# Kernel tuning notes

Measured on AMD Instinct MI355X. Metric: run time of the kernel, lower is better.

The kernel has to match this reference:

```python
import jax, jax.numpy as jnp
import numpy as np

N_NODES = 100000
N_EDGES = 3200000
FEAT = 64
N_GRAPHS = 64


def setup_inputs() -> dict:
    key = jax.random.key(0)
    ks = jax.random.split(key, 6)
    x = jax.random.normal(ks[0], (N_NODES, FEAT), dtype=jnp.float32)
    edge_index = jax.random.randint(ks[1], (2, N_EDGES), 0, N_NODES, dtype=jnp.int64)
    batch = jnp.sort(jax.random.randint(ks[2], (N_NODES,), 0, N_GRAPHS, dtype=jnp.int64))
    W1 = jax.random.normal(ks[3], (FEAT, FEAT), dtype=jnp.float32) * 0.1
    b1 = jnp.zeros((FEAT,), dtype=jnp.float32)
    W2 = jax.random.normal(ks[4], (FEAT, FEAT), dtype=jnp.float32) * 0.1
    b2 = jnp.zeros((FEAT,), dtype=jnp.float32)
    return {"x": x, "edge_index": edge_index, "batch": batch,
            "W1": W1, "b1": b1, "W2": W2, "b2": b2}


def _gcn_conv(x, W, b, row, col, n_nodes):
    # GCNConv: x' = D^{-1/2} (A + I) D^{-1/2} (x W) + b  (self-loops already in row/col)
    h = x @ W                                               # [N, F_out]
    deg = jax.ops.segment_sum(jnp.ones_like(col, dtype=h.dtype), col,
                              num_segments=n_nodes)         # [N]
    dinv = jnp.where(deg > 0, jax.lax.rsqrt(deg), 0.0)
    norm = dinv[row] * dinv[col]                            # [E+N]
    msgs = h[row] * norm[:, None]                           # gather + scale  [E+N, F]
    out = jax.ops.segment_sum(msgs, col, num_segments=n_nodes)  # scatter-add
    return out + b


def reference(x, edge_index, batch, W1, b1, W2, b2):
    n_nodes = x.shape[0]
    # add self-loops (PyG GCNConv default)
    loop = jnp.arange(n_nodes, dtype=edge_index.dtype)
    row = jnp.concatenate([edge_index[0], loop])
    col = jnp.concatenate([edge_index[1], loop])

    h = _gcn_conv(x, W1, b1, row, col, n_nodes)
    h = jax.nn.relu(h)
    # dropout is identity in eval mode (deterministic reference)
    h = _gcn_conv(h, W2, b2, row, col, n_nodes)
    h = jax.nn.relu(h)

    # global mean pool over graphs in the batch
    sums = jax.ops.segment_sum(h, batch, num_segments=N_GRAPHS)          # [G, F]
    counts = jax.ops.segment_sum(jnp.ones((n_nodes,), h.dtype), batch,
                                 num_segments=N_GRAPHS)                  # [G]
    return sums / jnp.maximum(counts, 1.0)[:, None]
```

## Files before the change

kernel.cpp:

```cpp
#include <hip/hip_runtime.h>

#define N_NODES 100000
#define N_EDGES 3200000
#define FEAT 64
#define N_GRAPHS 64

#define BKT_SHIFT 8
#define BKT_SIZE  256
#define NBKT      391
#define BKT_PAD   8960
#define E4        (N_EDGES / 4)
#define GEMM1_BLKS ((N_NODES + 63) / 64)

__device__ __forceinline__ ushort f2bf(float f) {
    unsigned u = __float_as_uint(f);
    return (ushort)((u + 0x7fffu + ((u >> 16) & 1u)) >> 16);
}
__device__ __forceinline__ float bf2f(ushort s) {
    return __uint_as_float(((unsigned)s) << 16);
}

__global__ void k_zero(int* __restrict__ bcnt, float* __restrict__ pool, int* __restrict__ offs) {
    int i = blockIdx.x * blockDim.x + threadIdx.x;
    if (i < NBKT) bcnt[i] = 0;
    if (i < N_GRAPHS * FEAT + N_GRAPHS) pool[i] = 0.0f;
    if (i == 0) offs[N_NODES] = N_EDGES;
}

__global__ void __launch_bounds__(1024) k_pre(const int* __restrict__ row,
                                              const int* __restrict__ col,
                                              int* __restrict__ bcnt,
                                              int* __restrict__ tmp,
                                              const float* __restrict__ x,
                                              const float* __restrict__ W1,
                                              ushort* __restrict__ hbf) {
    __shared__ int lcnt0[NBKT];
    __shared__ int lcnt1[NBKT];
    __shared__ float Ws[64][64];
    __shared__ float At[64][68];
    int tid = threadIdx.x;

    if (blockIdx.x < 196) {
        int* lc = (tid >= 512) ? lcnt1 : lcnt0;
        if (tid < NBKT) { lcnt0[tid] = 0; lcnt1[tid] = 0; }
        __syncthreads();
        int base = blockIdx.x * 4096;
        int4 c[4];
        #pragma unroll
        for (int k = 0; k < 4; ++k) {
            int t4 = base + k * 1024 + tid;
            if (t4 < E4) {
                c[k] = ((const int4*)col)[t4];
                atomicAdd(&lc[c[k].x >> BKT_SHIFT], 1);
                atomicAdd(&lc[c[k].y >> BKT_SHIFT], 1);
                atomicAdd(&lc[c[k].z >> BKT_SHIFT], 1);
                atomicAdd(&lc[c[k].w >> BKT_SHIFT], 1);
            }
        }
        __syncthreads();
        if (tid < NBKT) {
            int l0 = lcnt0[tid], l1 = lcnt1[tid];
            int bse = atomicAdd(&bcnt[tid], l0 + l1);
            lcnt0[tid] = bse;
            lcnt1[tid] = bse + l0;
        }
        __syncthreads();
        #pragma unroll
        for (int k = 0; k < 4; ++k) {
            int t4 = base + k * 1024 + tid;
            if (t4 < E4) {
                int4 r = ((const int4*)row)[t4];
                int b0 = c[k].x >> BKT_SHIFT, b1 = c[k].y >> BKT_SHIFT;
                int b2 = c[k].z >> BKT_SHIFT, b3 = c[k].w >> BKT_SHIFT;
                int s0 = atomicAdd(&lc[b0], 1);
                int s1 = atomicAdd(&lc[b1], 1);
                int s2 = atomicAdd(&lc[b2], 1);
                int s3 = atomicAdd(&lc[b3], 1);
                if (s0 < BKT_PAD) tmp[b0 * BKT_PAD + s0] = (r.x << BKT_SHIFT) | (c[k].x & (BKT_SIZE - 1));
                if (s1 < BKT_PAD) tmp[b1 * BKT_PAD + s1] = (r.y << BKT_SHIFT) | (c[k].y & (BKT_SIZE - 1));
                if (s2 < BKT_PAD) tmp[b2 * BKT_PAD + s2] = (r.z << BKT_SHIFT) | (c[k].z & (BKT_SIZE - 1));
                if (s3 < BKT_PAD) tmp[b3 * BKT_PAD + s3] = (r.w << BKT_SHIFT) | (c[k].w & (BKT_SIZE - 1));
            }
        }
    } else {
        int row0 = (blockIdx.x - 196) * 64;
        {
            float4 v = ((const float4*)W1)[tid];
            *(float4*)&Ws[tid >> 4][(tid & 15) * 4] = v;
        }
        {
            int r = tid >> 4, f4 = tid & 15;
            int grow = row0 + r;
            float4 v = make_float4(0.f, 0.f, 0.f, 0.f);
            if (grow < N_NODES) v = ((const float4*)(x + (size_t)grow * FEAT))[f4];
            int k = f4 * 4;
            At[k][r] = v.x; At[k + 1][r] = v.y; At[k + 2][r] = v.z; At[k + 3][r] = v.w;
        }
        __syncthreads();
        int tx = tid & 31, ty = tid >> 5;
        float a00 = 0.f, a01 = 0.f, a10 = 0.f, a11 = 0.f;
        #pragma unroll 8
        for (int k = 0; k < 64; ++k) {
            float2 wv = *(const float2*)&Ws[k][tx * 2];
            float2 av = *(const float2*)&At[k][ty * 2];
            a00 = fmaf(av.x, wv.x, a00); a01 = fmaf(av.x, wv.y, a01);
            a10 = fmaf(av.y, wv.x, a10); a11 = fmaf(av.y, wv.y, a11);
        }
        int r0 = row0 + ty * 2;
        if (r0 < N_NODES)
            *(unsigned*)(hbf + (size_t)r0 * FEAT + tx * 2) =
                (unsigned)f2bf(a00) | ((unsigned)f2bf(a01) << 16);
        if (r0 + 1 < N_NODES)
            *(unsigned*)(hbf + (size_t)(r0 + 1) * FEAT + tx * 2) =
                (unsigned)f2bf(a10) | ((unsigned)f2bf(a11) << 16);
    }
}

__global__ void __launch_bounds__(1024) k_build(const int* __restrict__ tmp,
                                                const int* __restrict__ bcnt,
                                                int* __restrict__ offs,
                                                float* __restrict__ dinv,
                                                int* __restrict__ csr_row) {
    __shared__ int hist[BKT_SIZE];
    __shared__ int wpart[4];
    __shared__ int sh_start;
    int b = blockIdx.x, tid = threadIdx.x;

    if (tid < 64) {
        int sum = 0;
        for (int c = 0; c < NBKT; c += 64) {
            int idx = c + tid;
            int v = (idx < b) ? bcnt[idx] : 0;
            #pragma unroll
            for (int d2 = 1; d2 < 64; d2 <<= 1) v += __shfl_xor(v, d2);
            sum += v;
        }
        if (tid == 0) sh_start = sum;
    }
    if (tid < BKT_SIZE) hist[tid] = 0;
    __syncthreads();
    int s = sh_start;
    int count = min(bcnt[b], BKT_PAD);
    const int* seg = tmp + (size_t)b * BKT_PAD;

    int e[9];
    #pragma unroll
    for (int k = 0; k < 9; ++k) {
        int idx = k * 1024 + tid;
        e[k] = -1;
        if (idx < count) {
            e[k] = seg[idx];
            atomicAdd(&hist[e[k] & (BKT_SIZE - 1)], 1);
        }
    }
    __syncthreads();

    int cnt_n = 0, p = 0;
    if (tid < BKT_SIZE) {
        cnt_n = hist[tid];
        p = cnt_n;
        #pragma unroll
        for (int d = 1; d < 64; d <<= 1) {
            int t2 = __shfl_up(p, d);
            if ((tid & 63) >= d) p += t2;
        }
        if ((tid & 63) == 63) wpart[tid >> 6] = p;
    }
    __syncthreads();
    if (tid == 0) {
        int run = 0;
        #pragma unroll
        for (int w = 0; w < 4; ++w) { int t2 = wpart[w]; wpart[w] = run; run += t2; }
    }
    __syncthreads();
    if (tid < BKT_SIZE) {
        int excl = wpart[tid >> 6] + p - cnt_n;
        int node = (b << BKT_SHIFT) + tid;
        if (node < N_NODES) {
            offs[node] = s + excl;
            dinv[node] = rsqrtf((float)(cnt_n + 1));
        }
        hist[tid] = s + excl;
    }
    __syncthreads();

    #pragma unroll
    for (int k = 0; k < 9; ++k) {
        if (e[k] >= 0) {
            int slot = atomicAdd(&hist[e[k] & (BKT_SIZE - 1)], 1);
            csr_row[slot] = e[k] >> BKT_SHIFT;
        }
    }
}

__global__ void __launch_bounds__(256, 4) k_gemm2(const ushort* __restrict__ in,
                                                  const float* __restrict__ W,
                                                  const float* __restrict__ bias,
                                                  const float* __restrict__ dinv,
                                                  ushort* __restrict__ out) {
    __shared__ float Ws[64][64];
    __shared__ float At[64][68];
    int tid = threadIdx.x;
    int row0 = blockIdx.x * 64;

    const float4* Wv = (const float4*)W;
    #pragma unroll
    for (int i = 0; i < 4; ++i) {
        int idx = tid + i * 256;
        float4 v = Wv[idx];
        *(float4*)&Ws[idx >> 4][(idx & 15) * 4] = v;
    }
    #pragma unroll
    for (int i = 0; i < 2; ++i) {
        int idx = tid + i * 256;
        int r = idx >> 3, q = idx & 7;
        int grow = row0 + r;
        uint4 v = make_uint4(0u, 0u, 0u, 0u);
        if (grow < N_NODES) v = ((const uint4*)(in + (size_t)grow * FEAT))[q];
        float4 b0 = ((const float4*)bias)[q * 2];
        float4 b1 = ((const float4*)bias)[q * 2 + 1];
        int k = q * 8;
        At[k + 0][r] = fmaxf(__uint_as_float(v.x << 16)          + b0.x, 0.f);
        At[k + 1][r] = fmaxf(__uint_as_float(v.x & 0xffff0000u)  + b0.y, 0.f);
        At[k + 2][r] = fmaxf(__uint_as_float(v.y << 16)          + b0.z, 0.f);
        At[k + 3][r] = fmaxf(__uint_as_float(v.y & 0xffff0000u)  + b0.w, 0.f);
        At[k + 4][r] = fmaxf(__uint_as_float(v.z << 16)          + b1.x, 0.f);
        At[k + 5][r] = fmaxf(__uint_as_float(v.z & 0xffff0000u)  + b1.y, 0.f);
        At[k + 6][r] = fmaxf(__uint_as_float(v.w << 16)          + b1.z, 0.f);
        At[k + 7][r] = fmaxf(__uint_as_float(v.w & 0xffff0000u)  + b1.w, 0.f);
    }
    __syncthreads();

    int tx = tid & 15, ty = tid >> 4;
    float acc[4][4] = {};
    #pragma unroll 8
    for (int k = 0; k < 64; ++k) {
        float4 wv = *(const float4*)&Ws[k][tx * 4];
        float4 av = *(const float4*)&At[k][ty * 4];
        acc[0][0] = fmaf(av.x, wv.x, acc[0][0]); acc[0][1] = fmaf(av.x, wv.y, acc[0][1]);
        acc[0][2] = fmaf(av.x, wv.z, acc[0][2]); acc[0][3] = fmaf(av.x, wv.w, acc[0][3]);
        acc[1][0] = fmaf(av.y, wv.x, acc[1][0]); acc[1][1] = fmaf(av.y, wv.y, acc[1][1]);
        acc[1][2] = fmaf(av.y, wv.z, acc[1][2]); acc[1][3] = fmaf(av.y, wv.w, acc[1][3]);
        acc[2][0] = fmaf(av.z, wv.x, acc[2][0]); acc[2][1] = fmaf(av.z, wv.y, acc[2][1]);
        acc[2][2] = fmaf(av.z, wv.z, acc[2][2]); acc[2][3] = fmaf(av.z, wv.w, acc[2][3]);
        acc[3][0] = fmaf(av.w, wv.x, acc[3][0]); acc[3][1] = fmaf(av.w, wv.y, acc[3][1]);
        acc[3][2] = fmaf(av.w, wv.z, acc[3][2]); acc[3][3] = fmaf(av.w, wv.w, acc[3][3]);
    }
    #pragma unroll
    for (int i = 0; i < 4; ++i) {
        int r = row0 + ty * 4 + i;
        if (r < N_NODES) {
            float d = dinv[r];
            ushort4 o;
            o.x = f2bf(acc[i][0] * d);
            o.y = f2bf(acc[i][1] * d);
            o.z = f2bf(acc[i][2] * d);
            o.w = f2bf(acc[i][3] * d);
            *(ushort4*)(out + (size_t)r * FEAT + tx * 4) = o;
        }
    }
}

template <bool SRC_SCALED>
__global__ void k_gather(const ushort* __restrict__ h, const float* __restrict__ dinv,
                         const int* __restrict__ off, const int* __restrict__ csr_row,
                         ushort* __restrict__ out) {
    int tid = threadIdx.x;
    int lane = tid & 63;
    int node = blockIdx.x * (blockDim.x >> 6) + (tid >> 6);
    if (node >= N_NODES) return;
    int g = lane >> 3;
    int sl = lane & 7;
    int s = off[node], e = off[node + 1];
    float a0 = 0.f, a1 = 0.f, a2 = 0.f, a3 = 0.f, a4 = 0.f, a5 = 0.f, a6 = 0.f, a7 = 0.f;

#define ACC8(vv, wt) do {                                           \
        a0 = fmaf(__uint_as_float((vv).x << 16),         wt, a0);   \
        a1 = fmaf(__uint_as_float((vv).x & 0xffff0000u), wt, a1);   \
        a2 = fmaf(__uint_as_float((vv).y << 16),         wt, a2);   \
        a3 = fmaf(__uint_as_float((vv).y & 0xffff0000u), wt, a3);   \
        a4 = fmaf(__uint_as_float((vv).z << 16),         wt, a4);   \
        a5 = fmaf(__uint_as_float((vv).z & 0xffff0000u), wt, a5);   \
        a6 = fmaf(__uint_as_float((vv).w << 16),         wt, a6);   \
        a7 = fmaf(__uint_as_float((vv).w & 0xffff0000u), wt, a7);   \
    } while (0)

    float selfw = SRC_SCALED ? 1.0f : dinv[node];
    if (g == 0) {
        uint4 v = ((const uint4*)(h + (size_t)node * FEAT))[sl];
        ACC8(v, selfw);
    }
    int base = s;
    for (; base + 32 <= e; base += 32) {
        int r0 = csr_row[base + g];
        int r1 = csr_row[base + 8 + g];
        int r2 = csr_row[base + 16 + g];
        int r3 = csr_row[base + 24 + g];
        float w0 = SRC_SCALED ? 1.0f : dinv[r0];
        float w1 = SRC_SCALED ? 1.0f : dinv[r1];
        float w2 = SRC_SCALED ? 1.0f : dinv[r2];
        float w3 = SRC_SCALED ? 1.0f : dinv[r3];
        uint4 v0 = ((const uint4*)(h + (size_t)r0 * FEAT))[sl];
        uint4 v1 = ((const uint4*)(h + (size_t)r1 * FEAT))[sl];
        uint4 v2 = ((const uint4*)(h + (size_t)r2 * FEAT))[sl];
        uint4 v3 = ((const uint4*)(h + (size_t)r3 * FEAT))[sl];
        ACC8(v0, w0); ACC8(v1, w1); ACC8(v2, w2); ACC8(v3, w3);
    }
    if (base + 16 <= e) {
        int r0 = csr_row[base + g];
        int r1 = csr_row[base + 8 + g];
        float w0 = SRC_SCALED ? 1.0f : dinv[r0];
        float w1 = SRC_SCALED ? 1.0f : dinv[r1];
        uint4 v0 = ((const uint4*)(h + (size_t)r0 * FEAT))[sl];
        uint4 v1 = ((const uint4*)(h + (size_t)r1 * FEAT))[sl];
        ACC8(v0, w0); ACC8(v1, w1);
        base += 16;
    }
    for (; base < e; base += 8) {
        int ei = base + g;
        if (ei < e) {
            int r = csr_row[ei];
            float wt = SRC_SCALED ? 1.0f : dinv[r];
            uint4 v = ((const uint4*)(h + (size_t)r * FEAT))[sl];
            ACC8(v, wt);
        }
    }
#undef ACC8
#define RED(a) a += __shfl_xor(a, 8); a += __shfl_xor(a, 16); a += __shfl_xor(a, 32);
    RED(a0) RED(a1) RED(a2) RED(a3) RED(a4) RED(a5) RED(a6) RED(a7)
#undef RED
    if (g == 0) {
        float d = dinv[node];
        uint4 o;
        o.x = (unsigned)f2bf(a0 * d) | ((unsigned)f2bf(a1 * d) << 16);
        o.y = (unsigned)f2bf(a2 * d) | ((unsigned)f2bf(a3 * d) << 16);
        o.z = (unsigned)f2bf(a4 * d) | ((unsigned)f2bf(a5 * d) << 16);
        o.w = (unsigned)f2bf(a6 * d) | ((unsigned)f2bf(a7 * d) << 16);
        ((uint4*)(out + (size_t)node * FEAT))[sl] = o;
    }
}

__global__ void k_pool(const ushort* __restrict__ agg, const float* __restrict__ b2,
                       const int* __restrict__ batch, float* sums, float* cnts) {
    const int NPB = 64;
    int f = threadIdx.x;
    int start = blockIdx.x * NPB;
    if (start >= N_NODES) return;
    int end = min(start + NPB, N_NODES);
    float bias = b2[f];
    int gcur = batch[start];
    float acc = 0.0f, cacc = 0.0f;
    for (int n = start; n < end; ++n) {
        int g = batch[n];
        if (g != gcur) {
            atomicAdd(&sums[gcur * FEAT + f], acc);
            if (f == 0) atomicAdd(&cnts[gcur], cacc);
            acc = 0.0f; cacc = 0.0f; gcur = g;
        }
        float v = bf2f(agg[(size_t)n * FEAT + f]) + bias;
        acc += fmaxf(v, 0.0f);
        cacc += 1.0f;
    }
    atomicAdd(&sums[gcur * FEAT + f], acc);
    if (f == 0) atomicAdd(&cnts[gcur], cacc);
}

__global__ void k_final(const float* __restrict__ sums, const float* __restrict__ cnts,
                        float* __restrict__ out) {
    int i = blockIdx.x * blockDim.x + threadIdx.x;
    if (i < N_GRAPHS * FEAT) out[i] = sums[i] / fmaxf(cnts[i >> 6], 1.0f);
}

extern "C" void kernel_launch(void* const* d_in, const int* in_sizes, int n_in,
                              void* d_out, int out_size, void* d_ws, size_t ws_size,
                              hipStream_t stream) {
    const float* x     = (const float*)d_in[0];
    const int*   ei    = (const int*)d_in[1];
    const int*   batch = (const int*)d_in[2];
    const float* W1    = (const float*)d_in[3];
    const float* b1    = (const float*)d_in[4];
    const float* W2    = (const float*)d_in[5];
    const float* b2    = (const float*)d_in[6];
    const int* row = ei;
    const int* col = ei + N_EDGES;

    size_t o = 0;
    auto alloc = [&](size_t bytes) { size_t cur = o; o = (o + bytes + 255) & ~(size_t)255; return cur; };
    char* ws = (char*)d_ws;
    float*  dinv    = (float*) (ws + alloc(N_NODES * 4));
    int*    offs    = (int*)   (ws + alloc((N_NODES + 1) * 4));
    int*    bcnt    = (int*)   (ws + alloc(NBKT * 4));
    float*  pool    = (float*) (ws + alloc((N_GRAPHS * FEAT + N_GRAPHS) * 4));
    ushort* hbf     = (ushort*)(ws + alloc((size_t)N_NODES * FEAT * 2));
    ushort* aggA    = (ushort*)(ws + alloc((size_t)N_NODES * FEAT * 2));
    ushort* aggB    = (ushort*)(ws + alloc((size_t)N_NODES * FEAT * 2));
    int*    csr_row = (int*)   (ws + alloc((size_t)N_EDGES * 4));
    int*    tmp     = (int*)   (ws + alloc((size_t)NBKT * BKT_PAD * 4));
    float* psum = pool;
    float* pcnt = pool + N_GRAPHS * FEAT;

    const int B = 256;
    hipLaunchKernelGGL(k_zero, dim3(17), dim3(B), 0, stream, bcnt, pool, offs);
    hipLaunchKernelGGL(k_pre, dim3(196 + GEMM1_BLKS), dim3(1024), 0, stream,
                       row, col, bcnt, tmp, x, W1, hbf);
    hipLaunchKernelGGL(k_build, dim3(NBKT), dim3(1024), 0, stream, tmp, bcnt, offs, dinv, csr_row);

    hipLaunchKernelGGL((k_gather<false>), dim3((N_NODES + 3) / 4), dim3(B), 0, stream,
                       hbf, dinv, offs, csr_row, aggA);
    hipLaunchKernelGGL(k_gemm2, dim3((N_NODES + 63) / 64), dim3(B), 0, stream, aggA, W2, b1, dinv, hbf);
    hipLaunchKernelGGL((k_gather<true>), dim3((N_NODES + 3) / 4), dim3(B), 0, stream,
                       hbf, dinv, offs, csr_row, aggB);

    hipLaunchKernelGGL(k_pool, dim3((N_NODES + 63) / 64), dim3(64), 0, stream, aggB, b2, batch, psum, pcnt);
    hipLaunchKernelGGL(k_final, dim3(16), dim3(B), 0, stream, psum, pcnt, (float*)d_out);
}
```

Before: 233.7 us.

## Split node features into four 16-column planes so gathers run per plane

Stores the bf16 hidden features in a planar layout of four 16-feature slices, each N_NODES×16. The gather kernel runs four passes, one plane per group of 25000 blocks, so each pass's working set (about 3.2MB) is more likely to stay in cache during random row gathers. The GEMM stores, the gemm2 loads and the pool reads are adjusted to the new layout. In exchange, each neighbor fetch shrinks to 8 bytes per lane, CSR indices and dinv are re-read four times, and the reductions take more shuffle steps.

```diff
diff --git a/kernel.cpp b/kernel.cpp
--- a/kernel.cpp
+++ b/kernel.cpp
@@ -11,6 +11,8 @@
 #define BKT_PAD   8960
 #define E4        (N_EDGES / 4)
 #define GEMM1_BLKS ((N_NODES + 63) / 64)
+#define PASS_BLKS 25000
+
 
 __device__ __forceinline__ ushort f2bf(float f) {
     unsigned u = __float_as_uint(f);
@@ -107,11 +109,13 @@
             a10 = fmaf(av.y, wv.x, a10); a11 = fmaf(av.y, wv.y, a11);
         }
         int r0 = row0 + ty * 2;
+        int p = tx >> 3;
+        int off16 = (tx * 2) & 15;
         if (r0 < N_NODES)
-            *(unsigned*)(hbf + (size_t)r0 * FEAT + tx * 2) =
+            *(unsigned*)(hbf + ((size_t)p * N_NODES + r0) * 16 + off16) =
                 (unsigned)f2bf(a00) | ((unsigned)f2bf(a01) << 16);
         if (r0 + 1 < N_NODES)
-            *(unsigned*)(hbf + (size_t)(r0 + 1) * FEAT + tx * 2) =
+            *(unsigned*)(hbf + ((size_t)p * N_NODES + r0 + 1) * 16 + off16) =
                 (unsigned)f2bf(a10) | ((unsigned)f2bf(a11) << 16);
     }
 }
@@ -216,7 +220,10 @@
         int r = idx >> 3, q = idx & 7;
         int grow = row0 + r;
         uint4 v = make_uint4(0u, 0u, 0u, 0u);
-        if (grow < N_NODES) v = ((const uint4*)(in + (size_t)grow * FEAT))[q];
+        if (grow < N_NODES) {
+            int p = q >> 1, off16 = (q & 1) * 8;
+            v = *(const uint4*)(in + ((size_t)p * N_NODES + grow) * 16 + off16);
+        }
         float4 b0 = ((const float4*)bias)[q * 2];
         float4 b1 = ((const float4*)bias)[q * 2 + 1];
         int k = q * 8;
@@ -246,6 +253,7 @@
         acc[3][0] = fmaf(av.w, wv.x, acc[3][0]); acc[3][1] = fmaf(av.w, wv.y, acc[3][1]);
         acc[3][2] = fmaf(av.w, wv.z, acc[3][2]); acc[3][3] = fmaf(av.w, wv.w, acc[3][3]);
     }
+    int p = tx >> 2, off16 = (tx * 4) & 15;
     #pragma unroll
     for (int i = 0; i < 4; ++i) {
         int r = row0 + ty * 4 + i;
@@ -256,87 +264,75 @@
             o.y = f2bf(acc[i][1] * d);
             o.z = f2bf(acc[i][2] * d);
             o.w = f2bf(acc[i][3] * d);
-            *(ushort4*)(out + (size_t)r * FEAT + tx * 4) = o;
+            *(ushort4*)(out + ((size_t)p * N_NODES + r) * 16 + off16) = o;
         }
     }
 }
 
 template <bool SRC_SCALED>
-__global__ void k_gather(const ushort* __restrict__ h, const float* __restrict__ dinv,
+__global__ void k_gather(const ushort* __restrict__ h,
+                         const float* __restrict__ dinv,
                          const int* __restrict__ off, const int* __restrict__ csr_row,
                          ushort* __restrict__ out) {
     int tid = threadIdx.x;
     int lane = tid & 63;
-    int node = blockIdx.x * (blockDim.x >> 6) + (tid >> 6);
-    if (node >= N_NODES) return;
-    int g = lane >> 3;
-    int sl = lane & 7;
+    int bid = blockIdx.x;
+    int pass = bid / PASS_BLKS;
+    int node = (bid - pass * PASS_BLKS) * 4 + (tid >> 6);
+    int g = lane >> 2;
+    int sl = lane & 3;
+    const ushort* hp = h + (size_t)pass * N_NODES * 16;
+    ushort* op = out + (size_t)pass * N_NODES * 16;
     int s = off[node], e = off[node + 1];
-    float a0 = 0.f, a1 = 0.f, a2 = 0.f, a3 = 0.f, a4 = 0.f, a5 = 0.f, a6 = 0.f, a7 = 0.f;
-
-#define ACC8(vv, wt) do {                                           \
+    float a0 = 0.f, a1 = 0.f, a2 = 0.f, a3 = 0.f;
+
+#define ACC4(vv, wt) do {                                           \
         a0 = fmaf(__uint_as_float((vv).x << 16),         wt, a0);   \
         a1 = fmaf(__uint_as_float((vv).x & 0xffff0000u), wt, a1);   \
         a2 = fmaf(__uint_as_float((vv).y << 16),         wt, a2);   \
         a3 = fmaf(__uint_as_float((vv).y & 0xffff0000u), wt, a3);   \
-        a4 = fmaf(__uint_as_float((vv).z << 16),         wt, a4);   \
-        a5 = fmaf(__uint_as_float((vv).z & 0xffff0000u), wt, a5);   \
-        a6 = fmaf(__uint_as_float((vv).w << 16),         wt, a6);   \
-        a7 = fmaf(__uint_as_float((vv).w & 0xffff0000u), wt, a7);   \
     } while (0)
 
-    float selfw = SRC_SCALED ? 1.0f : dinv[node];
     if (g == 0) {
-        uint4 v = ((const uint4*)(h + (size_t)node * FEAT))[sl];
-        ACC8(v, selfw);
+        uint2 v = ((const uint2*)(hp + (size_t)node * 16))[sl];
+        ACC4(v, SRC_SCALED ? 1.0f : dinv[node]);
     }
     int base = s;
     for (; base + 32 <= e; base += 32) {
         int r0 = csr_row[base + g];
-        int r1 = csr_row[base + 8 + g];
-        int r2 = csr_row[base + 16 + g];
-        int r3 = csr_row[base + 24 + g];
+        int r1 = csr_row[base + 16 + g];
         float w0 = SRC_SCALED ? 1.0f : dinv[r0];
         float w1 = SRC_SCALED ? 1.0f : dinv[r1];
-        float w2 = SRC_SCALED ? 1.0f : dinv[r2];
-        float w3 = SRC_SCALED ? 1.0f : dinv[r3];
-        uint4 v0 = ((const uint4*)(h + (size_t)r0 * FEAT))[sl];
-        uint4 v1 = ((const uint4*)(h + (size_t)r1 * FEAT))[sl];
-        uint4 v2 = ((const uint4*)(h + (size_t)r2 * FEAT))[sl];
-        uint4 v3 = ((const uint4*)(h + (size_t)r3 * FEAT))[sl];
-        ACC8(v0, w0); ACC8(v1, w1); ACC8(v2, w2); ACC8(v3, w3);
+        uint2 v0 = ((const uint2*)(hp + (size_t)r0 * 16))[sl];
+        uint2 v1 = ((const uint2*)(hp + (size_t)r1 * 16))[sl];
+        ACC4(v0, w0); ACC4(v1, w1);
     }
     if (base + 16 <= e) {
         int r0 = csr_row[base + g];
-        int r1 = csr_row[base + 8 + g];
         float w0 = SRC_SCALED ? 1.0f : dinv[r0];
-        float w1 = SRC_SCALED ? 1.0f : dinv[r1];
-        uint4 v0 = ((const uint4*)(h + (size_t)r0 * FEAT))[sl];
-        uint4 v1 = ((const uint4*)(h + (size_t)r1 * FEAT))[sl];
-        ACC8(v0, w0); ACC8(v1, w1);
+        uint2 v0 = ((const uint2*)(hp + (size_t)r0 * 16))[sl];
+        ACC4(v0, w0);
         base += 16;
     }
-    for (; base < e; base += 8) {
+    if (base < e) {
         int ei = base + g;
         if (ei < e) {
             int r = csr_row[ei];
             float wt = SRC_SCALED ? 1.0f : dinv[r];
-            uint4 v = ((const uint4*)(h + (size_t)r * FEAT))[sl];
-            ACC8(v, wt);
-        }
-    }
-#undef ACC8
-#define RED(a) a += __shfl_xor(a, 8); a += __shfl_xor(a, 16); a += __shfl_xor(a, 32);
-    RED(a0) RED(a1) RED(a2) RED(a3) RED(a4) RED(a5) RED(a6) RED(a7)
+            uint2 v = ((const uint2*)(hp + (size_t)r * 16))[sl];
+            ACC4(v, wt);
+        }
+    }
+#undef ACC4
+#define RED(a) a += __shfl_xor(a, 4); a += __shfl_xor(a, 8); a += __shfl_xor(a, 16); a += __shfl_xor(a, 32);
+    RED(a0) RED(a1) RED(a2) RED(a3)
 #undef RED
     if (g == 0) {
         float d = dinv[node];
-        uint4 o;
+        uint2 o;
         o.x = (unsigned)f2bf(a0 * d) | ((unsigned)f2bf(a1 * d) << 16);
         o.y = (unsigned)f2bf(a2 * d) | ((unsigned)f2bf(a3 * d) << 16);
-        o.z = (unsigned)f2bf(a4 * d) | ((unsigned)f2bf(a5 * d) << 16);
-        o.w = (unsigned)f2bf(a6 * d) | ((unsigned)f2bf(a7 * d) << 16);
-        ((uint4*)(out + (size_t)node * FEAT))[sl] = o;
+        ((uint2*)(op + (size_t)node * 16))[sl] = o;
     }
 }
 
@@ -348,6 +344,7 @@
     if (start >= N_NODES) return;
     int end = min(start + NPB, N_NODES);
     float bias = b2[f];
+    const ushort* ap = agg + (size_t)(f >> 4) * N_NODES * 16 + (f & 15);
     int gcur = batch[start];
     float acc = 0.0f, cacc = 0.0f;
     for (int n = start; n < end; ++n) {
@@ -357,7 +354,7 @@
             if (f == 0) atomicAdd(&cnts[gcur], cacc);
             acc = 0.0f; cacc = 0.0f; gcur = g;
         }
-        float v = bf2f(agg[(size_t)n * FEAT + f]) + bias;
+        float v = bf2f(ap[(size_t)n * 16]) + bias;
         acc += fmaxf(v, 0.0f);
         cacc += 1.0f;
     }
@@ -405,10 +402,10 @@
                        row, col, bcnt, tmp, x, W1, hbf);
     hipLaunchKernelGGL(k_build, dim3(NBKT), dim3(1024), 0, stream, tmp, bcnt, offs, dinv, csr_row);
 
-    hipLaunchKernelGGL((k_gather<false>), dim3((N_NODES + 3) / 4), dim3(B), 0, stream,
+    hipLaunchKernelGGL((k_gather<false>), dim3(4 * PASS_BLKS), dim3(B), 0, stream,
                        hbf, dinv, offs, csr_row, aggA);
     hipLaunchKernelGGL(k_gemm2, dim3((N_NODES + 63) / 64), dim3(B), 0, stream, aggA, W2, b1, dinv, hbf);
-    hipLaunchKernelGGL((k_gather<true>), dim3((N_NODES + 3) / 4), dim3(B), 0, stream,
+    hipLaunchKernelGGL((k_gather<true>), dim3(4 * PASS_BLKS), dim3(B), 0, stream,
                        hbf, dinv, offs, csr_row, aggB);
 
     hipLaunchKernelGGL(k_pool, dim3((N_NODES + 63) / 64), dim3(64), 0, stream, aggB, b2, batch, psum, pcnt);
```

Result: slower. 402.9 us (+72.4%).

## Fuse layer-2 GEMM into first gather epilogue and halve edge-bucketing block size

Applied to the files above, without the earlier changes.

Removes the separate k_gemm2 kernel: the first gather now applies bias, ReLU, the W2 matmul and dinv scaling per node in its epilogue. It uses wave shuffles to broadcast the aggregated features and a shared-memory copy of W2. This drops one kernel launch and a full bf16 intermediate round-trip through memory. The trade-off is that every gather block loads the 16KB W2 into LDS and does 64 serial FMAs per lane, which may lower occupancy. Separately, the bucketing phase of k_pre now uses 391 blocks that each handle 2048 int4s instead of 196 blocks handling 4096, for more parallelism.

```diff
diff --git a/kernel.cpp b/kernel.cpp
--- a/kernel.cpp
+++ b/kernel.cpp
@@ -40,14 +40,14 @@
     __shared__ float At[64][68];
     int tid = threadIdx.x;
 
-    if (blockIdx.x < 196) {
+    if (blockIdx.x < NBKT) {
         int* lc = (tid >= 512) ? lcnt1 : lcnt0;
         if (tid < NBKT) { lcnt0[tid] = 0; lcnt1[tid] = 0; }
         __syncthreads();
-        int base = blockIdx.x * 4096;
-        int4 c[4];
-        #pragma unroll
-        for (int k = 0; k < 4; ++k) {
+        int base = blockIdx.x * 2048;
+        int4 c[2];
+        #pragma unroll
+        for (int k = 0; k < 2; ++k) {
             int t4 = base + k * 1024 + tid;
             if (t4 < E4) {
                 c[k] = ((const int4*)col)[t4];
@@ -66,7 +66,7 @@
         }
         __syncthreads();
         #pragma unroll
-        for (int k = 0; k < 4; ++k) {
+        for (int k = 0; k < 2; ++k) {
             int t4 = base + k * 1024 + tid;
             if (t4 < E4) {
                 int4 r = ((const int4*)row)[t4];
@@ -83,7 +83,7 @@
             }
         }
     } else {
-        int row0 = (blockIdx.x - 196) * 64;
+        int row0 = (blockIdx.x - NBKT) * 64;
         {
             float4 v = ((const float4*)W1)[tid];
             *(float4*)&Ws[tid >> 4][(tid & 15) * 4] = v;
@@ -193,102 +193,46 @@
     }
 }
 
-__global__ void __launch_bounds__(256, 4) k_gemm2(const ushort* __restrict__ in,
-                                                  const float* __restrict__ W,
-                                                  const float* __restrict__ bias,
-                                                  const float* __restrict__ dinv,
-                                                  ushort* __restrict__ out) {
-    __shared__ float Ws[64][64];
-    __shared__ float At[64][68];
+template <bool SRC_SCALED, bool FUSE_GEMM2>
+__global__ void __launch_bounds__(256) k_gather(const ushort* __restrict__ h,
+                                                const float* __restrict__ dinv,
+                                                const int* __restrict__ off,
+                                                const int* __restrict__ csr_row,
+                                                const float* __restrict__ W2,
+                                                const float* __restrict__ b1,
+                                                ushort* __restrict__ out) {
+    __shared__ float Wl[FEAT * FEAT];
+    __shared__ float bl[FEAT];
     int tid = threadIdx.x;
-    int row0 = blockIdx.x * 64;
-
-    const float4* Wv = (const float4*)W;
-    #pragma unroll
-    for (int i = 0; i < 4; ++i) {
-        int idx = tid + i * 256;
-        float4 v = Wv[idx];
-        *(float4*)&Ws[idx >> 4][(idx & 15) * 4] = v;
-    }
-    #pragma unroll
-    for (int i = 0; i < 2; ++i) {
-        int idx = tid + i * 256;
-        int r = idx >> 3, q = idx & 7;
-        int grow = row0 + r;
-        uint4 v = make_uint4(0u, 0u, 0u, 0u);
-        if (grow < N_NODES) v = ((const uint4*)(in + (size_t)grow * FEAT))[q];
-        float4 b0 = ((const float4*)bias)[q * 2];
-        float4 b1 = ((const float4*)bias)[q * 2 + 1];
-        int k = q * 8;
-        At[k + 0][r] = fmaxf(__uint_as_float(v.x << 16)          + b0.x, 0.f);
-        At[k + 1][r] = fmaxf(__uint_as_float(v.x & 0xffff0000u)  + b0.y, 0.f);
-        At[k + 2][r] = fmaxf(__uint_as_float(v.y << 16)          + b0.z, 0.f);
-        At[k + 3][r] = fmaxf(__uint_as_float(v.y & 0xffff0000u)  + b0.w, 0.f);
-        At[k + 4][r] = fmaxf(__uint_as_float(v.z << 16)          + b1.x, 0.f);
-        At[k + 5][r] = fmaxf(__uint_as_float(v.z & 0xffff0000u)  + b1.y, 0.f);
-        At[k + 6][r] = fmaxf(__uint_as_float(v.w << 16)          + b1.z, 0.f);
-        At[k + 7][r] = fmaxf(__uint_as_float(v.w & 0xffff0000u)  + b1.w, 0.f);
-    }
-    __syncthreads();
-
-    int tx = tid & 15, ty = tid >> 4;
-    float acc[4][4] = {};
-    #pragma unroll 8
-    for (int k = 0; k < 64; ++k) {
-        float4 wv = *(const float4*)&Ws[k][tx * 4];
-        float4 av = *(const float4*)&At[k][ty * 4];
-        acc[0][0] = fmaf(av.x, wv.x, acc[0][0]); acc[0][1] = fmaf(av.x, wv.y, acc[0][1]);
-        acc[0][2] = fmaf(av.x, wv.z, acc[0][2]); acc[0][3] = fmaf(av.x, wv.w, acc[0][3]);
-        acc[1][0] = fmaf(av.y, wv.x, acc[1][0]); acc[1][1] = fmaf(av.y, wv.y, acc[1][1]);
-        acc[1][2] = fmaf(av.y, wv.z, acc[1][2]); acc[1][3] = fmaf(av.y, wv.w, acc[1][3]);
-        acc[2][0] = fmaf(av.z, wv.x, acc[2][0]); acc[2][1] = fmaf(av.z, wv.y, acc[2][1]);
-        acc[2][2] = fmaf(av.z, wv.z, acc[2][2]); acc[2][3] = fmaf(av.z, wv.w, acc[2][3]);
-        acc[3][0] = fmaf(av.w, wv.x, acc[3][0]); acc[3][1] = fmaf(av.w, wv.y, acc[3][1]);
-        acc[3][2] = fmaf(av.w, wv.z, acc[3][2]); acc[3][3] = fmaf(av.w, wv.w, acc[3][3]);
-    }
-    #pragma unroll
-    for (int i = 0; i < 4; ++i) {
-        int r = row0 + ty * 4 + i;
-        if (r < N_NODES) {
-            float d = dinv[r];
-            ushort4 o;
-            o.x = f2bf(acc[i][0] * d);
-            o.y = f2bf(acc[i][1] * d);
-            o.z = f2bf(acc[i][2] * d);
-            o.w = f2bf(acc[i][3] * d);
-            *(ushort4*)(out + (size_t)r * FEAT + tx * 4) = o;
-        }
-    }
-}
-
-template <bool SRC_SCALED>
-__global__ void k_gather(const ushort* __restrict__ h, const float* __restrict__ dinv,
-                         const int* __restrict__ off, const int* __restrict__ csr_row,
-                         ushort* __restrict__ out) {
-    int tid = threadIdx.x;
+    if (FUSE_GEMM2) {
+        #pragma unroll
+        for (int i = 0; i < 4; ++i)
+            ((float4*)Wl)[tid + i * 256] = ((const float4*)W2)[tid + i * 256];
+        if (tid < FEAT) bl[tid] = b1[tid];
+        __syncthreads();
+    }
     int lane = tid & 63;
     int node = blockIdx.x * (blockDim.x >> 6) + (tid >> 6);
     if (node >= N_NODES) return;
     int g = lane >> 3;
     int sl = lane & 7;
     int s = off[node], e = off[node + 1];
-    float a0 = 0.f, a1 = 0.f, a2 = 0.f, a3 = 0.f, a4 = 0.f, a5 = 0.f, a6 = 0.f, a7 = 0.f;
-
-#define ACC8(vv, wt) do {                                           \
-        a0 = fmaf(__uint_as_float((vv).x << 16),         wt, a0);   \
-        a1 = fmaf(__uint_as_float((vv).x & 0xffff0000u), wt, a1);   \
-        a2 = fmaf(__uint_as_float((vv).y << 16),         wt, a2);   \
-        a3 = fmaf(__uint_as_float((vv).y & 0xffff0000u), wt, a3);   \
-        a4 = fmaf(__uint_as_float((vv).z << 16),         wt, a4);   \
-        a5 = fmaf(__uint_as_float((vv).z & 0xffff0000u), wt, a5);   \
-        a6 = fmaf(__uint_as_float((vv).w << 16),         wt, a6);   \
-        a7 = fmaf(__uint_as_float((vv).w & 0xffff0000u), wt, a7);   \
+    float a[8] = {};
+
+#define ACC8(vv, wt) do {                                              \
+        a[0] = fmaf(__uint_as_float((vv).x << 16),         wt, a[0]);  \
+        a[1] = fmaf(__uint_as_float((vv).x & 0xffff0000u), wt, a[1]);  \
+        a[2] = fmaf(__uint_as_float((vv).y << 16),         wt, a[2]);  \
+        a[3] = fmaf(__uint_as_float((vv).y & 0xffff0000u), wt, a[3]);  \
+        a[4] = fmaf(__uint_as_float((vv).z << 16),         wt, a[4]);  \
+        a[5] = fmaf(__uint_as_float((vv).z & 0xffff0000u), wt, a[5]);  \
+        a[6] = fmaf(__uint_as_float((vv).w << 16),         wt, a[6]);  \
+        a[7] = fmaf(__uint_as_float((vv).w & 0xffff0000u), wt, a[7]);  \
     } while (0)
 
-    float selfw = SRC_SCALED ? 1.0f : dinv[node];
     if (g == 0) {
         uint4 v = ((const uint4*)(h + (size_t)node * FEAT))[sl];
-        ACC8(v, selfw);
+        ACC8(v, SRC_SCALED ? 1.0f : dinv[node]);
     }
     int base = s;
     for (; base + 32 <= e; base += 32) {
@@ -326,16 +270,28 @@
         }
     }
 #undef ACC8
-#define RED(a) a += __shfl_xor(a, 8); a += __shfl_xor(a, 16); a += __shfl_xor(a, 32);
-    RED(a0) RED(a1) RED(a2) RED(a3) RED(a4) RED(a5) RED(a6) RED(a7)
-#undef RED
-    if (g == 0) {
-        float d = dinv[node];
+    #pragma unroll
+    for (int j = 0; j < 8; ++j) {
+        a[j] += __shfl_xor(a[j], 8);
+        a[j] += __shfl_xor(a[j], 16);
+        a[j] += __shfl_xor(a[j], 32);
+    }
+    float d = dinv[node];
+    if (FUSE_GEMM2) {
+        float acc = 0.0f;
+        #pragma unroll
+        for (int k = 0; k < 64; ++k) {
+            float rv = __shfl(a[k & 7], k >> 3);
+            float val = fmaxf(fmaf(rv, d, bl[k]), 0.0f);
+            acc = fmaf(val, Wl[k * FEAT + lane], acc);
+        }
+        out[(size_t)node * FEAT + lane] = f2bf(acc * d);
+    } else if (g == 0) {
         uint4 o;
-        o.x = (unsigned)f2bf(a0 * d) | ((unsigned)f2bf(a1 * d) << 16);
-        o.y = (unsigned)f2bf(a2 * d) | ((unsigned)f2bf(a3 * d) << 16);
-        o.z = (unsigned)f2bf(a4 * d) | ((unsigned)f2bf(a5 * d) << 16);
-        o.w = (unsigned)f2bf(a6 * d) | ((unsigned)f2bf(a7 * d) << 16);
+        o.x = (unsigned)f2bf(a[0] * d) | ((unsigned)f2bf(a[1] * d) << 16);
+        o.y = (unsigned)f2bf(a[2] * d) | ((unsigned)f2bf(a[3] * d) << 16);
+        o.z = (unsigned)f2bf(a[4] * d) | ((unsigned)f2bf(a[5] * d) << 16);
+        o.w = (unsigned)f2bf(a[6] * d) | ((unsigned)f2bf(a[7] * d) << 16);
         ((uint4*)(out + (size_t)node * FEAT))[sl] = o;
     }
 }
@@ -392,7 +348,7 @@
     int*    bcnt    = (int*)   (ws + alloc(NBKT * 4));
     float*  pool    = (float*) (ws + alloc((N_GRAPHS * FEAT + N_GRAPHS) * 4));
     ushort* hbf     = (ushort*)(ws + alloc((size_t)N_NODES * FEAT * 2));
-    ushort* aggA    = (ushort*)(ws + alloc((size_t)N_NODES * FEAT * 2));
+    ushort* h2bf    = (ushort*)(ws + alloc((size_t)N_NODES * FEAT * 2));
     ushort* aggB    = (ushort*)(ws + alloc((size_t)N_NODES * FEAT * 2));
     int*    csr_row = (int*)   (ws + alloc((size_t)N_EDGES * 4));
     int*    tmp     = (int*)   (ws + alloc((size_t)NBKT * BKT_PAD * 4));
@@ -401,15 +357,14 @@
 
     const int B = 256;
     hipLaunchKernelGGL(k_zero, dim3(17), dim3(B), 0, stream, bcnt, pool, offs);
-    hipLaunchKernelGGL(k_pre, dim3(196 + GEMM1_BLKS), dim3(1024), 0, stream,
+    hipLaunchKernelGGL(k_pre, dim3(NBKT + GEMM1_BLKS), dim3(1024), 0, stream,
                        row, col, bcnt, tmp, x, W1, hbf);
     hipLaunchKernelGGL(k_build, dim3(NBKT), dim3(1024), 0, stream, tmp, bcnt, offs, dinv, csr_row);
 
-    hipLaunchKernelGGL((k_gather<false>), dim3((N_NODES + 3) / 4), dim3(B), 0, stream,
-                       hbf, dinv, offs, csr_row, aggA);
-    hipLaunchKernelGGL(k_gemm2, dim3((N_NODES + 63) / 64), dim3(B), 0, stream, aggA, W2, b1, dinv, hbf);
-    hipLaunchKernelGGL((k_gather<true>), dim3((N_NODES + 3) / 4), dim3(B), 0, stream,
-                       hbf, dinv, offs, csr_row, aggB);
+    hipLaunchKernelGGL((k_gather<false, true>), dim3((N_NODES + 3) / 4), dim3(B), 0, stream,
+                       hbf, dinv, offs, csr_row, W2, b1, h2bf);
+    hipLaunchKernelGGL((k_gather<true, false>), dim3((N_NODES + 3) / 4), dim3(B), 0, stream,
+                       h2bf, dinv, offs, csr_row, W2, b1, aggB);
 
     hipLaunchKernelGGL(k_pool, dim3((N_NODES + 63) / 64), dim3(64), 0, stream, aggB, b2, batch, psum, pcnt);
     hipLaunchKernelGGL(k_final, dim3(16), dim3(B), 0, stream, psum, pcnt, (float*)d_out);
```

Measured after the change: 306.5 us. +31.1%, slower.
